# Performance work log

Hardware: AMD Instinct MI355X
Metric: run time of the kernel (lower is better)

## Reference

```python
import jax, jax.numpy as jnp
import numpy as np

B, C, F_, T = 32, 2, 1024, 512
CF = C * F_
H = 128  # lstm hidden / embedding dim


def setup_inputs() -> dict:
    key = jax.random.key(0)
    ks = jax.random.split(key, 12)
    s = 0.05
    return {
        "x": jax.random.normal(ks[0], (B, C, F_, T), dtype=jnp.float32),
        "W_fc1": jax.random.normal(ks[1], (H, CF), dtype=jnp.float32) * s,
        "b_fc1": jax.random.normal(ks[2], (H,), dtype=jnp.float32) * s,
        "Wih_f": jax.random.normal(ks[3], (4 * H, H), dtype=jnp.float32) * s,
        "Whh_f": jax.random.normal(ks[4], (4 * H, H), dtype=jnp.float32) * s,
        "b_f": jax.random.normal(ks[5], (4 * H,), dtype=jnp.float32) * s,
        "Wih_b": jax.random.normal(ks[6], (4 * H, H), dtype=jnp.float32) * s,
        "Whh_b": jax.random.normal(ks[7], (4 * H, H), dtype=jnp.float32) * s,
        "b_b": jax.random.normal(ks[8], (4 * H,), dtype=jnp.float32) * s,
        "W_out": jax.random.normal(ks[9], (H, 2 * H), dtype=jnp.float32) * s,
        "b_out": jax.random.normal(ks[10], (H,), dtype=jnp.float32) * s,
    }


def _lstm_scan(x, Wih, Whh, b):
    # x: (L, T, H); recurrence over L (torch treats the (B,128) input as an
    # unbatched sequence of length B), vectorized over the T frames.
    L, Tn, _ = x.shape
    Hn = Whh.shape[1]

    def step(carry, xt):
        h, c = carry  # (T, H)
        z = xt @ Wih.T + h @ Whh.T + b  # (T, 4H)
        i, f, g, o = jnp.split(z, 4, axis=-1)
        c = jax.nn.sigmoid(f) * c + jax.nn.sigmoid(i) * jnp.tanh(g)
        h = jax.nn.sigmoid(o) * jnp.tanh(c)
        return (h, c), h

    init = (jnp.zeros((Tn, Hn), x.dtype), jnp.zeros((Tn, Hn), x.dtype))
    _, hs = jax.lax.scan(step, init, x)
    return hs  # (L, T, H)


def reference(x, W_fc1, b_fc1, Wih_f, Whh_f, b_f, Wih_b, Whh_b, b_b, W_out, b_out):
    Bn, Cn, Fn, Tn = x.shape
    # fc1 applied per time frame: (B, CF, T) -> (B, T, 128)
    xr = x.reshape(Bn, Cn * Fn, Tn).transpose(0, 2, 1)
    h = jnp.einsum("btc,dc->btd", xr, W_fc1) + b_fc1
    # bidirectional LSTM over the batch axis (torch unbatched-input semantics)
    hf = _lstm_scan(h, Wih_f, Whh_f, b_f)
    hb = _lstm_scan(h[::-1], Wih_b, Whh_b, b_b)[::-1]
    hs = jnp.concatenate([hf, hb], axis=-1)  # (B, T, 256)
    out = jnp.einsum("btd,ed->bte", hs, W_out) + b_out  # (B, T, 128)
    return out.transpose(0, 2, 1)  # (B, 128, T), matching torch.stack(dim=2)
```

## Files before the change

kernel.cpp:

```cpp
#include <hip/hip_runtime.h>
#include <stdint.h>

typedef __attribute__((ext_vector_type(8))) short short8;
typedef __attribute__((ext_vector_type(4))) float floatx4;

__device__ __forceinline__ float bf16_to_f(uint16_t u) {
    union { uint32_t i; float f; } v; v.i = ((uint32_t)u) << 16; return v.f;
}
__device__ __forceinline__ uint16_t f_to_bf16(float f) {
    union { uint32_t i; float f; } v; v.f = f;
    uint32_t u = v.i;
    u += 0x7FFFu + ((u >> 16) & 1u);
    return (uint16_t)(u >> 16);
}
__device__ __forceinline__ void gload16(const void* g, void* l) {
    __builtin_amdgcn_global_load_lds(
        (const __attribute__((address_space(1))) void*)g,
        (__attribute__((address_space(3))) void*)l, 16, 0, 0);
}
__device__ __forceinline__ float rcpf(float x) { return __builtin_amdgcn_rcpf(x); }

#define B_  32
#define T_  512
#define CF_ 2048
#define H_  128
#define G4_ 512
#define LOG2E 1.4426950408889634f

__device__ __forceinline__ void gemm64(const uint16_t* __restrict__ A,
                                       const uint16_t* __restrict__ B,
                                       int K, uint16_t* As, uint16_t* Bs,
                                       floatx4 acc[2][2]) {
    const int tid = threadIdx.x, w = tid >> 6, l = tid & 63;
    const int wm = (w >> 1) * 32, wn = (w & 1) * 32;
    const int lm = l & 15, lk = l >> 4;
    const uint16_t* gA = A + (size_t)l * K;
    const uint16_t* gB = B + (size_t)l * K;
    uint16_t* dA0 = As + ((2 * w) * 64 + l) * 8;
    uint16_t* dA1 = As + ((2 * w + 1) * 64 + l) * 8;
    uint16_t* dB0 = Bs + ((2 * w) * 64 + l) * 8;
    uint16_t* dB1 = Bs + ((2 * w + 1) * 64 + l) * 8;
    for (int k0 = 0; k0 < K; k0 += 64) {
        __syncthreads();
        gload16(gA + k0 + (2 * w) * 8,     dA0);
        gload16(gA + k0 + (2 * w + 1) * 8, dA1);
        gload16(gB + k0 + (2 * w) * 8,     dB0);
        gload16(gB + k0 + (2 * w + 1) * 8, dB1);
        __syncthreads();
        short8 a[2][2], b[2][2];
        #pragma unroll
        for (int kf = 0; kf < 2; ++kf) {
            #pragma unroll
            for (int mf = 0; mf < 2; ++mf)
                a[mf][kf] = *(const short8*)&As[(size_t)((kf * 4 + lk) * 64 + wm + mf * 16 + lm) * 8];
            #pragma unroll
            for (int nf = 0; nf < 2; ++nf)
                b[nf][kf] = *(const short8*)&Bs[(size_t)((kf * 4 + lk) * 64 + wn + nf * 16 + lm) * 8];
        }
        #pragma unroll
        for (int mf = 0; mf < 2; ++mf)
            #pragma unroll
            for (int nf = 0; nf < 2; ++nf) {
                acc[mf][nf] = __builtin_amdgcn_mfma_f32_16x16x32_bf16(a[mf][0], b[nf][0], acc[mf][nf], 0, 0, 0);
                acc[mf][nf] = __builtin_amdgcn_mfma_f32_16x16x32_bf16(a[mf][1], b[nf][1], acc[mf][nf], 0, 0, 0);
            }
    }
}

__global__ __launch_bounds__(256) void k_cvt_all(
        const float* __restrict__ Wfc, const float* __restrict__ Wih_f,
        const float* __restrict__ Wih_b, const float* __restrict__ Whh_f,
        const float* __restrict__ Whh_b, const float* __restrict__ Wout,
        uint16_t* __restrict__ WfcB, uint16_t* __restrict__ WihB,
        uint16_t* __restrict__ WhhB, uint16_t* __restrict__ WoutB) {
    const int blk = blockIdx.x;
    const float* s; uint16_t* d; int off;
    if (blk < 256)      { s = Wfc;   d = WfcB;          off = blk; }
    else if (blk < 320) { s = Wih_f; d = WihB;          off = blk - 256; }
    else if (blk < 384) { s = Wih_b; d = WihB + 65536;  off = blk - 320; }
    else if (blk < 448) { s = Whh_f; d = WhhB;          off = blk - 384; }
    else if (blk < 512) { s = Whh_b; d = WhhB + 65536;  off = blk - 448; }
    else                { s = Wout;  d = WoutB;         off = blk - 512; }
    const int i = off * 1024 + threadIdx.x * 4;
    float4 v = *(const float4*)&s[i];
    ushort4 o;
    o.x = f_to_bf16(v.x); o.y = f_to_bf16(v.y);
    o.z = f_to_bf16(v.z); o.w = f_to_bf16(v.w);
    *(ushort4*)&d[i] = o;
}

__global__ __launch_bounds__(256) void k_xt(const float* __restrict__ x,
                                            uint16_t* __restrict__ xT) {
    __shared__ float tile[64][65];
    const int b = blockIdx.z, cf0 = blockIdx.y * 64, t0 = blockIdx.x * 64;
    const int tid = threadIdx.x;
    #pragma unroll
    for (int p = 0; p < 4; ++p) {
        int cf_r = p * 16 + (tid >> 4);
        int t4   = (tid & 15) * 4;
        float4 v = *(const float4*)&x[((size_t)b * CF_ + cf0 + cf_r) * T_ + t0 + t4];
        tile[t4 + 0][cf_r] = v.x; tile[t4 + 1][cf_r] = v.y;
        tile[t4 + 2][cf_r] = v.z; tile[t4 + 3][cf_r] = v.w;
    }
    __syncthreads();
    #pragma unroll
    for (int p = 0; p < 4; ++p) {
        int t_r = p * 16 + (tid >> 4);
        int cf4 = (tid & 15) * 4;
        ushort4 o;
        o.x = f_to_bf16(tile[t_r][cf4 + 0]);
        o.y = f_to_bf16(tile[t_r][cf4 + 1]);
        o.z = f_to_bf16(tile[t_r][cf4 + 2]);
        o.w = f_to_bf16(tile[t_r][cf4 + 3]);
        *(ushort4*)&xT[((size_t)b * T_ + t0 + t_r) * CF_ + cf0 + cf4] = o;
    }
}

__global__ __launch_bounds__(256) void k_fc1m(const uint16_t* __restrict__ Wb,
                                              const uint16_t* __restrict__ xT,
                                              const float* __restrict__ bfc,
                                              uint16_t* __restrict__ Hfc) {
    __shared__ __align__(16) uint16_t As[4096], Bs[4096];
    const int b = blockIdx.z, m0 = blockIdx.y * 64, n0 = blockIdx.x * 64;
    floatx4 acc[2][2] = {};
    gemm64(Wb + (size_t)m0 * CF_, xT + ((size_t)b * T_ + n0) * CF_, CF_, As, Bs, acc);
    const int tid = threadIdx.x, w = tid >> 6, l = tid & 63;
    const int wm = (w >> 1) * 32, wn = (w & 1) * 32, lm = l & 15, lk = l >> 4;
    #pragma unroll
    for (int mf = 0; mf < 2; ++mf) {
        const int d0 = m0 + wm + mf * 16 + lk * 4;
        const float4 bv = *(const float4*)&bfc[d0];
        #pragma unroll
        for (int nf = 0; nf < 2; ++nf) {
            const int t = n0 + wn + nf * 16 + lm;
            ushort4 o;
            o.x = f_to_bf16(acc[mf][nf][0] + bv.x);
            o.y = f_to_bf16(acc[mf][nf][1] + bv.y);
            o.z = f_to_bf16(acc[mf][nf][2] + bv.z);
            o.w = f_to_bf16(acc[mf][nf][3] + bv.w);
            *(ushort4*)&Hfc[((size_t)b * T_ + t) * H_ + d0] = o;
        }
    }
}

__global__ __launch_bounds__(256) void k_xprojm(const uint16_t* __restrict__ WihB,
                                                const float* __restrict__ b_f,
                                                const float* __restrict__ b_b,
                                                const uint16_t* __restrict__ Hfc,
                                                uint16_t* __restrict__ Xp) {
    __shared__ __align__(16) uint16_t As[4096], Bs[4096];
    const int db = blockIdx.z, dir = db >> 5, b = db & 31;
    const int g0 = blockIdx.y * 64, n0 = blockIdx.x * 64;
    const float* bi = dir ? b_b : b_f;
    floatx4 acc[2][2] = {};
    gemm64(WihB + ((size_t)dir * G4_ + g0) * H_, Hfc + ((size_t)b * T_ + n0) * H_, H_, As, Bs, acc);
    const int tid = threadIdx.x, w = tid >> 6, l = tid & 63;
    const int wm = (w >> 1) * 32, wn = (w & 1) * 32, lm = l & 15, lk = l >> 4;
    #pragma unroll
    for (int mf = 0; mf < 2; ++mf) {
        const int g_ = g0 + wm + mf * 16 + lk * 4;
        const float4 bv = *(const float4*)&bi[g_];
        #pragma unroll
        for (int nf = 0; nf < 2; ++nf) {
            const int t = n0 + wn + nf * 16 + lm;
            ushort4 o;
            o.x = f_to_bf16(acc[mf][nf][0] + bv.x);
            o.y = f_to_bf16(acc[mf][nf][1] + bv.y);
            o.z = f_to_bf16(acc[mf][nf][2] + bv.z);
            o.w = f_to_bf16(acc[mf][nf][3] + bv.w);
            *(ushort4*)&Xp[((size_t)db * T_ + t) * G4_ + g_] = o;
        }
    }
}

__global__ __launch_bounds__(512) void k_lstm(const uint16_t* __restrict__ Xp,
                                              const uint16_t* __restrict__ WhhB,
                                              uint16_t* __restrict__ hs) {
    __shared__ __align__(16) uint16_t h_sh[16 * 136];
    __shared__ float z_sh[16 * 516];
    const int dir = blockIdx.y, t0 = blockIdx.x * 16;
    const int tid = threadIdx.x, w = tid >> 6, l = tid & 63;
    const int lm = l & 15, lk = l >> 4;
    const int gw = w * 64;
    const uint16_t* Wp = WhhB + dir * (G4_ * H_);

    short8 bw[4][4];
    #pragma unroll
    for (int nf = 0; nf < 4; ++nf)
        #pragma unroll
        for (int kf = 0; kf < 4; ++kf)
            bw[nf][kf] = *(const short8*)&Wp[(size_t)(gw + nf * 16 + lm) * H_ + kf * 32 + lk * 8];

    for (int i = tid; i < 16 * 136; i += 512) h_sh[i] = 0;
    const int hh = tid & 127, tq = tid >> 7;
    float c[4] = {0.f, 0.f, 0.f, 0.f};
    __syncthreads();

    for (int s = 0; s < 32; ++s) {
        const int b_idx = dir ? (31 - s) : s;
        const uint16_t* xp = Xp + ((size_t)(dir * B_ + b_idx) * T_ + t0) * G4_;
        uint16_t xv[4][4];
        #pragma unroll
        for (int j = 0; j < 4; ++j)
            #pragma unroll
            for (int gg = 0; gg < 4; ++gg)
                xv[j][gg] = xp[(size_t)(tq * 4 + j) * G4_ + gg * H_ + hh];

        short8 af[4];
        #pragma unroll
        for (int kf = 0; kf < 4; ++kf)
            af[kf] = *(const short8*)&h_sh[lm * 136 + kf * 32 + lk * 8];
        floatx4 acc[4] = {};
        #pragma unroll
        for (int nf = 0; nf < 4; ++nf)
            #pragma unroll
            for (int kf = 0; kf < 4; ++kf)
                acc[nf] = __builtin_amdgcn_mfma_f32_16x16x32_bf16(af[kf], bw[nf][kf], acc[nf], 0, 0, 0);
        #pragma unroll
        for (int nf = 0; nf < 4; ++nf)
            #pragma unroll
            for (int r = 0; r < 4; ++r)
                z_sh[(lk * 4 + r) * 516 + gw + nf * 16 + lm] = acc[nf][r];
        __syncthreads();

        #pragma unroll
        for (int j = 0; j < 4; ++j) {
            const int t = tq * 4 + j;
            const float* zr = &z_sh[t * 516];
            float zi = zr[hh]            + bf16_to_f(xv[j][0]);
            float zf = zr[H_ + hh]       + bf16_to_f(xv[j][1]);
            float zg = zr[2 * H_ + hh]   + bf16_to_f(xv[j][2]);
            float zo = zr[3 * H_ + hh]   + bf16_to_f(xv[j][3]);
            float si = rcpf(1.f + __builtin_amdgcn_exp2f(-LOG2E * zi));
            float sf = rcpf(1.f + __builtin_amdgcn_exp2f(-LOG2E * zf));
            float so = rcpf(1.f + __builtin_amdgcn_exp2f(-LOG2E * zo));
            float tg = 1.f - 2.f * rcpf(1.f + __builtin_amdgcn_exp2f(2.f * LOG2E * zg));
            c[j] = sf * c[j] + si * tg;
            float tc = 1.f - 2.f * rcpf(1.f + __builtin_amdgcn_exp2f(2.f * LOG2E * c[j]));
            float hn = so * tc;
            uint16_t hb = f_to_bf16(hn);
            h_sh[t * 136 + hh] = hb;
            hs[((size_t)b_idx * T_ + t0 + t) * 256 + dir * H_ + hh] = hb;
        }
        __syncthreads();
    }
}

__global__ __launch_bounds__(256) void k_outm(const uint16_t* __restrict__ WoutB,
                                              const uint16_t* __restrict__ hs,
                                              const float* __restrict__ bout,
                                              float* __restrict__ out) {
    __shared__ __align__(16) uint16_t As[4096], Bs[4096];
    const int b = blockIdx.z, m0 = blockIdx.y * 64, n0 = blockIdx.x * 64;
    floatx4 acc[2][2] = {};
    gemm64(WoutB + (size_t)m0 * 256, hs + ((size_t)b * T_ + n0) * 256, 256, As, Bs, acc);
    const int tid = threadIdx.x, w = tid >> 6, l = tid & 63;
    const int wm = (w >> 1) * 32, wn = (w & 1) * 32, lm = l & 15, lk = l >> 4;
    #pragma unroll
    for (int mf = 0; mf < 2; ++mf) {
        const int e0 = m0 + wm + mf * 16 + lk * 4;
        const float4 bv = *(const float4*)&bout[e0];
        #pragma unroll
        for (int nf = 0; nf < 2; ++nf) {
            const int t = n0 + wn + nf * 16 + lm;
            out[((size_t)b * H_ + e0 + 0) * T_ + t] = acc[mf][nf][0] + bv.x;
            out[((size_t)b * H_ + e0 + 1) * T_ + t] = acc[mf][nf][1] + bv.y;
            out[((size_t)b * H_ + e0 + 2) * T_ + t] = acc[mf][nf][2] + bv.z;
            out[((size_t)b * H_ + e0 + 3) * T_ + t] = acc[mf][nf][3] + bv.w;
        }
    }
}

extern "C" void kernel_launch(void* const* d_in, const int* in_sizes, int n_in,
                              void* d_out, int out_size, void* d_ws, size_t ws_size,
                              hipStream_t stream) {
    const float* x     = (const float*)d_in[0];
    const float* Wfc   = (const float*)d_in[1];
    const float* bfc   = (const float*)d_in[2];
    const float* Wih_f = (const float*)d_in[3];
    const float* Whh_f = (const float*)d_in[4];
    const float* b_f   = (const float*)d_in[5];
    const float* Wih_b = (const float*)d_in[6];
    const float* Whh_b = (const float*)d_in[7];
    const float* b_b   = (const float*)d_in[8];
    const float* Wout  = (const float*)d_in[9];
    const float* bout  = (const float*)d_in[10];
    float* out = (float*)d_out;

    char* ws = (char*)d_ws;
    uint16_t* xT    = (uint16_t*)(ws);
    uint16_t* HfcB  = (uint16_t*)(ws + 67108864);
    uint16_t* Xp    = (uint16_t*)(ws + 75497472);
    uint16_t* hsB   = (uint16_t*)(ws + 109051904);
    uint16_t* WfcB  = (uint16_t*)(ws + 117440512);
    uint16_t* WihB  = (uint16_t*)(ws + 117964800);
    uint16_t* WhhB  = (uint16_t*)(ws + 118226944);
    uint16_t* WoutB = (uint16_t*)(ws + 118489088);

    k_cvt_all<<<dim3(544), 256, 0, stream>>>(Wfc, Wih_f, Wih_b, Whh_f, Whh_b, Wout,
                                             WfcB, WihB, WhhB, WoutB);
    k_xt    <<<dim3(8, 32, 32), 256, 0, stream>>>(x, xT);
    k_fc1m  <<<dim3(8, 2, 32),  256, 0, stream>>>(WfcB, xT, bfc, HfcB);
    k_xprojm<<<dim3(8, 8, 64),  256, 0, stream>>>(WihB, b_f, b_b, HfcB, Xp);
    k_lstm  <<<dim3(32, 2),     512, 0, stream>>>(Xp, WhhB, hsB);
    k_outm  <<<dim3(8, 2, 32),  256, 0, stream>>>(WoutB, hsB, bout, out);
}
```

Before: 341.6 us.

## Fuse x transpose, fc1 GEMM and LSTM input projection into one kernel

```diff
diff --git a/kernel.cpp b/kernel.cpp
--- a/kernel.cpp
+++ b/kernel.cpp
@@ -26,46 +26,6 @@
 #define H_  128
 #define G4_ 512
 #define LOG2E 1.4426950408889634f
-
-__device__ __forceinline__ void gemm64(const uint16_t* __restrict__ A,
-                                       const uint16_t* __restrict__ B,
-                                       int K, uint16_t* As, uint16_t* Bs,
-                                       floatx4 acc[2][2]) {
-    const int tid = threadIdx.x, w = tid >> 6, l = tid & 63;
-    const int wm = (w >> 1) * 32, wn = (w & 1) * 32;
-    const int lm = l & 15, lk = l >> 4;
-    const uint16_t* gA = A + (size_t)l * K;
-    const uint16_t* gB = B + (size_t)l * K;
-    uint16_t* dA0 = As + ((2 * w) * 64 + l) * 8;
-    uint16_t* dA1 = As + ((2 * w + 1) * 64 + l) * 8;
-    uint16_t* dB0 = Bs + ((2 * w) * 64 + l) * 8;
-    uint16_t* dB1 = Bs + ((2 * w + 1) * 64 + l) * 8;
-    for (int k0 = 0; k0 < K; k0 += 64) {
-        __syncthreads();
-        gload16(gA + k0 + (2 * w) * 8,     dA0);
-        gload16(gA + k0 + (2 * w + 1) * 8, dA1);
-        gload16(gB + k0 + (2 * w) * 8,     dB0);
-        gload16(gB + k0 + (2 * w + 1) * 8, dB1);
-        __syncthreads();
-        short8 a[2][2], b[2][2];
-        #pragma unroll
-        for (int kf = 0; kf < 2; ++kf) {
-            #pragma unroll
-            for (int mf = 0; mf < 2; ++mf)
-                a[mf][kf] = *(const short8*)&As[(size_t)((kf * 4 + lk) * 64 + wm + mf * 16 + lm) * 8];
-            #pragma unroll
-            for (int nf = 0; nf < 2; ++nf)
-                b[nf][kf] = *(const short8*)&Bs[(size_t)((kf * 4 + lk) * 64 + wn + nf * 16 + lm) * 8];
-        }
-        #pragma unroll
-        for (int mf = 0; mf < 2; ++mf)
-            #pragma unroll
-            for (int nf = 0; nf < 2; ++nf) {
-                acc[mf][nf] = __builtin_amdgcn_mfma_f32_16x16x32_bf16(a[mf][0], b[nf][0], acc[mf][nf], 0, 0, 0);
-                acc[mf][nf] = __builtin_amdgcn_mfma_f32_16x16x32_bf16(a[mf][1], b[nf][1], acc[mf][nf], 0, 0, 0);
-            }
-    }
-}
 
 __global__ __launch_bounds__(256) void k_cvt_all(
         const float* __restrict__ Wfc, const float* __restrict__ Wih_f,
@@ -89,86 +49,141 @@
     *(ushort4*)&d[i] = o;
 }
 
-__global__ __launch_bounds__(256) void k_xt(const float* __restrict__ x,
-                                            uint16_t* __restrict__ xT) {
-    __shared__ float tile[64][65];
-    const int b = blockIdx.z, cf0 = blockIdx.y * 64, t0 = blockIdx.x * 64;
-    const int tid = threadIdx.x;
-    #pragma unroll
-    for (int p = 0; p < 4; ++p) {
-        int cf_r = p * 16 + (tid >> 4);
-        int t4   = (tid & 15) * 4;
-        float4 v = *(const float4*)&x[((size_t)b * CF_ + cf0 + cf_r) * T_ + t0 + t4];
-        tile[t4 + 0][cf_r] = v.x; tile[t4 + 1][cf_r] = v.y;
-        tile[t4 + 2][cf_r] = v.z; tile[t4 + 3][cf_r] = v.w;
+__global__ __launch_bounds__(512) void k_fc1x(const float* __restrict__ x,
+                                              const uint16_t* __restrict__ WfcB,
+                                              const float* __restrict__ bfc,
+                                              const uint16_t* __restrict__ WihB,
+                                              const float* __restrict__ b_f,
+                                              const float* __restrict__ b_b,
+                                              uint16_t* __restrict__ Xp) {
+    __shared__ float tile[64 * 65];
+    __shared__ __align__(16) uint16_t As[8192];
+    __shared__ __align__(16) uint16_t Bs[4224];
+    __shared__ __align__(16) uint16_t Hs2[8432];
+
+    const int bb = blockIdx.y, n0 = blockIdx.x * 64;
+    const int tid = threadIdx.x, w = tid >> 6, l = tid & 63;
+    const int lm = l & 15, lk = l >> 4;
+    const float* xb = x + (size_t)bb * CF_ * T_;
+
+    const int t4 = (tid & 15) * 4, cf_r = tid >> 4;
+    const int kk = (tid & 15) * 4, t_r = tid >> 4;
+
+    float4 xv0, xv1;
+    {
+        const float* p = &xb[(size_t)(0 + cf_r) * T_ + n0 + t4];
+        xv0 = *(const float4*)p;
+        xv1 = *(const float4*)(p + 32 * T_);
+    }
+
+    const int wmA = (w >> 1) * 32, wnA = (w & 1) * 32;
+    floatx4 acc[2][2] = {};
+    for (int k0 = 0; k0 < CF_; k0 += 64) {
+        __syncthreads();
+        tile[(t4 + 0) * 65 + cf_r] = xv0.x;
+        tile[(t4 + 1) * 65 + cf_r] = xv0.y;
+        tile[(t4 + 2) * 65 + cf_r] = xv0.z;
+        tile[(t4 + 3) * 65 + cf_r] = xv0.w;
+        tile[(t4 + 0) * 65 + cf_r + 32] = xv1.x;
+        tile[(t4 + 1) * 65 + cf_r + 32] = xv1.y;
+        tile[(t4 + 2) * 65 + cf_r + 32] = xv1.z;
+        tile[(t4 + 3) * 65 + cf_r + 32] = xv1.w;
+        gload16(WfcB + (size_t)l * CF_ + k0 + w * 8,        As + (w * 128 + l) * 8);
+        gload16(WfcB + (size_t)(64 + l) * CF_ + k0 + w * 8, As + (w * 128 + 64 + l) * 8);
+        __syncthreads();
+        if (k0 + 64 < CF_) {
+            const float* p = &xb[(size_t)(k0 + 64 + cf_r) * T_ + n0 + t4];
+            xv0 = *(const float4*)p;
+            xv1 = *(const float4*)(p + 32 * T_);
+        }
+        #pragma unroll
+        for (int pass = 0; pass < 2; ++pass) {
+            const int tr = t_r + pass * 32;
+            ushort4 o;
+            o.x = f_to_bf16(tile[tr * 65 + kk + 0]);
+            o.y = f_to_bf16(tile[tr * 65 + kk + 1]);
+            o.z = f_to_bf16(tile[tr * 65 + kk + 2]);
+            o.w = f_to_bf16(tile[tr * 65 + kk + 3]);
+            *(ushort4*)&Bs[((kk >> 3) * 66 + tr) * 8 + (kk & 7)] = o;
+        }
+        __syncthreads();
+        short8 a[2][2], bfr[2][2];
+        #pragma unroll
+        for (int kf = 0; kf < 2; ++kf) {
+            #pragma unroll
+            for (int mf = 0; mf < 2; ++mf)
+                a[mf][kf] = *(const short8*)&As[((kf * 4 + lk) * 128 + wmA + mf * 16 + lm) * 8];
+            #pragma unroll
+            for (int nf = 0; nf < 2; ++nf)
+                bfr[nf][kf] = *(const short8*)&Bs[((kf * 4 + lk) * 66 + wnA + nf * 16 + lm) * 8];
+        }
+        #pragma unroll
+        for (int mf = 0; mf < 2; ++mf)
+            #pragma unroll
+            for (int nf = 0; nf < 2; ++nf) {
+                acc[mf][nf] = __builtin_amdgcn_mfma_f32_16x16x32_bf16(a[mf][0], bfr[nf][0], acc[mf][nf], 0, 0, 0);
+                acc[mf][nf] = __builtin_amdgcn_mfma_f32_16x16x32_bf16(a[mf][1], bfr[nf][1], acc[mf][nf], 0, 0, 0);
+            }
     }
     __syncthreads();
     #pragma unroll
-    for (int p = 0; p < 4; ++p) {
-        int t_r = p * 16 + (tid >> 4);
-        int cf4 = (tid & 15) * 4;
-        ushort4 o;
-        o.x = f_to_bf16(tile[t_r][cf4 + 0]);
-        o.y = f_to_bf16(tile[t_r][cf4 + 1]);
-        o.z = f_to_bf16(tile[t_r][cf4 + 2]);
-        o.w = f_to_bf16(tile[t_r][cf4 + 3]);
-        *(ushort4*)&xT[((size_t)b * T_ + t0 + t_r) * CF_ + cf0 + cf4] = o;
-    }
-}
-
-__global__ __launch_bounds__(256) void k_fc1m(const uint16_t* __restrict__ Wb,
-                                              const uint16_t* __restrict__ xT,
-                                              const float* __restrict__ bfc,
-                                              uint16_t* __restrict__ Hfc) {
-    __shared__ __align__(16) uint16_t As[4096], Bs[4096];
-    const int b = blockIdx.z, m0 = blockIdx.y * 64, n0 = blockIdx.x * 64;
-    floatx4 acc[2][2] = {};
-    gemm64(Wb + (size_t)m0 * CF_, xT + ((size_t)b * T_ + n0) * CF_, CF_, As, Bs, acc);
-    const int tid = threadIdx.x, w = tid >> 6, l = tid & 63;
-    const int wm = (w >> 1) * 32, wn = (w & 1) * 32, lm = l & 15, lk = l >> 4;
-    #pragma unroll
     for (int mf = 0; mf < 2; ++mf) {
-        const int d0 = m0 + wm + mf * 16 + lk * 4;
+        const int d0 = wmA + mf * 16 + lk * 4;
         const float4 bv = *(const float4*)&bfc[d0];
+        const int c = ((wmA + mf * 16) >> 3) + (lk >> 1);
         #pragma unroll
         for (int nf = 0; nf < 2; ++nf) {
-            const int t = n0 + wn + nf * 16 + lm;
+            const int t = wnA + nf * 16 + lm;
             ushort4 o;
             o.x = f_to_bf16(acc[mf][nf][0] + bv.x);
             o.y = f_to_bf16(acc[mf][nf][1] + bv.y);
             o.z = f_to_bf16(acc[mf][nf][2] + bv.z);
             o.w = f_to_bf16(acc[mf][nf][3] + bv.w);
-            *(ushort4*)&Hfc[((size_t)b * T_ + t) * H_ + d0] = o;
-        }
-    }
-}
-
-__global__ __launch_bounds__(256) void k_xprojm(const uint16_t* __restrict__ WihB,
-                                                const float* __restrict__ b_f,
-                                                const float* __restrict__ b_b,
-                                                const uint16_t* __restrict__ Hfc,
-                                                uint16_t* __restrict__ Xp) {
-    __shared__ __align__(16) uint16_t As[4096], Bs[4096];
-    const int db = blockIdx.z, dir = db >> 5, b = db & 31;
-    const int g0 = blockIdx.y * 64, n0 = blockIdx.x * 64;
-    const float* bi = dir ? b_b : b_f;
-    floatx4 acc[2][2] = {};
-    gemm64(WihB + ((size_t)dir * G4_ + g0) * H_, Hfc + ((size_t)b * T_ + n0) * H_, H_, As, Bs, acc);
-    const int tid = threadIdx.x, w = tid >> 6, l = tid & 63;
-    const int wm = (w >> 1) * 32, wn = (w & 1) * 32, lm = l & 15, lk = l >> 4;
+            *(ushort4*)&Hs2[(c * 66 + t) * 8 + (lk & 1) * 4] = o;
+        }
+    }
+    __syncthreads();
+
+    const int dirw = w >> 2;
+    const int db   = dirw * B_ + bb;
+    const uint16_t* Wp = WihB + (size_t)dirw * (G4_ * H_);
+    const float* bi = dirw ? b_b : b_f;
     #pragma unroll
-    for (int mf = 0; mf < 2; ++mf) {
-        const int g_ = g0 + wm + mf * 16 + lk * 4;
-        const float4 bv = *(const float4*)&bi[g_];
-        #pragma unroll
-        for (int nf = 0; nf < 2; ++nf) {
-            const int t = n0 + wn + nf * 16 + lm;
-            ushort4 o;
-            o.x = f_to_bf16(acc[mf][nf][0] + bv.x);
-            o.y = f_to_bf16(acc[mf][nf][1] + bv.y);
-            o.z = f_to_bf16(acc[mf][nf][2] + bv.z);
-            o.w = f_to_bf16(acc[mf][nf][3] + bv.w);
-            *(ushort4*)&Xp[((size_t)db * T_ + t) * G4_ + g_] = o;
+    for (int it = 0; it < 2; ++it) {
+        const int gbase = (w & 3) * 64 + it * 256;
+        short8 aw[4][4];
+        #pragma unroll
+        for (int mf = 0; mf < 4; ++mf)
+            #pragma unroll
+            for (int kf = 0; kf < 4; ++kf)
+                aw[mf][kf] = *(const short8*)&Wp[(size_t)(gbase + mf * 16 + lm) * H_ + kf * 32 + lk * 8];
+        floatx4 acc2[4][4] = {};
+        #pragma unroll
+        for (int nf = 0; nf < 4; ++nf) {
+            short8 bbf[4];
+            #pragma unroll
+            for (int kf = 0; kf < 4; ++kf)
+                bbf[kf] = *(const short8*)&Hs2[((kf * 4 + lk) * 66 + nf * 16 + lm) * 8];
+            #pragma unroll
+            for (int mf = 0; mf < 4; ++mf)
+                #pragma unroll
+                for (int kf = 0; kf < 4; ++kf)
+                    acc2[mf][nf] = __builtin_amdgcn_mfma_f32_16x16x32_bf16(aw[mf][kf], bbf[kf], acc2[mf][nf], 0, 0, 0);
+        }
+        #pragma unroll
+        for (int mf = 0; mf < 4; ++mf) {
+            const int g0 = gbase + mf * 16 + lk * 4;
+            const float4 bv = *(const float4*)&bi[g0];
+            #pragma unroll
+            for (int nf = 0; nf < 4; ++nf) {
+                const int t = n0 + nf * 16 + lm;
+                ushort4 o;
+                o.x = f_to_bf16(acc2[mf][nf][0] + bv.x);
+                o.y = f_to_bf16(acc2[mf][nf][1] + bv.y);
+                o.z = f_to_bf16(acc2[mf][nf][2] + bv.z);
+                o.w = f_to_bf16(acc2[mf][nf][3] + bv.w);
+                *(ushort4*)&Xp[((size_t)db * T_ + t) * G4_ + g0] = o;
+            }
         }
     }
 }
@@ -252,10 +267,39 @@
                                               float* __restrict__ out) {
     __shared__ __align__(16) uint16_t As[4096], Bs[4096];
     const int b = blockIdx.z, m0 = blockIdx.y * 64, n0 = blockIdx.x * 64;
+    const int tid = threadIdx.x, w = tid >> 6, l = tid & 63;
+    const int wm = (w >> 1) * 32, wn = (w & 1) * 32;
+    const int lm = l & 15, lk = l >> 4;
+    const uint16_t* A = WoutB + (size_t)m0 * 256;
+    const uint16_t* Bp = hs + ((size_t)b * T_ + n0) * 256;
     floatx4 acc[2][2] = {};
-    gemm64(WoutB + (size_t)m0 * 256, hs + ((size_t)b * T_ + n0) * 256, 256, As, Bs, acc);
-    const int tid = threadIdx.x, w = tid >> 6, l = tid & 63;
-    const int wm = (w >> 1) * 32, wn = (w & 1) * 32, lm = l & 15, lk = l >> 4;
+    const uint16_t* gA = A + (size_t)l * 256;
+    const uint16_t* gB = Bp + (size_t)l * 256;
+    for (int k0 = 0; k0 < 256; k0 += 64) {
+        __syncthreads();
+        gload16(gA + k0 + (2 * w) * 8,     As + ((2 * w) * 64 + l) * 8);
+        gload16(gA + k0 + (2 * w + 1) * 8, As + ((2 * w + 1) * 64 + l) * 8);
+        gload16(gB + k0 + (2 * w) * 8,     Bs + ((2 * w) * 64 + l) * 8);
+        gload16(gB + k0 + (2 * w + 1) * 8, Bs + ((2 * w + 1) * 64 + l) * 8);
+        __syncthreads();
+        short8 a[2][2], bfr[2][2];
+        #pragma unroll
+        for (int kf = 0; kf < 2; ++kf) {
+            #pragma unroll
+            for (int mf = 0; mf < 2; ++mf)
+                a[mf][kf] = *(const short8*)&As[((kf * 4 + lk) * 64 + wm + mf * 16 + lm) * 8];
+            #pragma unroll
+            for (int nf = 0; nf < 2; ++nf)
+                bfr[nf][kf] = *(const short8*)&Bs[((kf * 4 + lk) * 64 + wn + nf * 16 + lm) * 8];
+        }
+        #pragma unroll
+        for (int mf = 0; mf < 2; ++mf)
+            #pragma unroll
+            for (int nf = 0; nf < 2; ++nf) {
+                acc[mf][nf] = __builtin_amdgcn_mfma_f32_16x16x32_bf16(a[mf][0], bfr[nf][0], acc[mf][nf], 0, 0, 0);
+                acc[mf][nf] = __builtin_amdgcn_mfma_f32_16x16x32_bf16(a[mf][1], bfr[nf][1], acc[mf][nf], 0, 0, 0);
+            }
+    }
     #pragma unroll
     for (int mf = 0; mf < 2; ++mf) {
         const int e0 = m0 + wm + mf * 16 + lk * 4;
@@ -288,20 +332,16 @@
     float* out = (float*)d_out;
 
     char* ws = (char*)d_ws;
-    uint16_t* xT    = (uint16_t*)(ws);
-    uint16_t* HfcB  = (uint16_t*)(ws + 67108864);
-    uint16_t* Xp    = (uint16_t*)(ws + 75497472);
-    uint16_t* hsB   = (uint16_t*)(ws + 109051904);
-    uint16_t* WfcB  = (uint16_t*)(ws + 117440512);
-    uint16_t* WihB  = (uint16_t*)(ws + 117964800);
-    uint16_t* WhhB  = (uint16_t*)(ws + 118226944);
-    uint16_t* WoutB = (uint16_t*)(ws + 118489088);
+    uint16_t* Xp    = (uint16_t*)(ws);
+    uint16_t* hsB   = (uint16_t*)(ws + 33554432);
+    uint16_t* WfcB  = (uint16_t*)(ws + 41943040);
+    uint16_t* WihB  = (uint16_t*)(ws + 42467328);
+    uint16_t* WhhB  = (uint16_t*)(ws + 42729472);
+    uint16_t* WoutB = (uint16_t*)(ws + 42991616);
 
     k_cvt_all<<<dim3(544), 256, 0, stream>>>(Wfc, Wih_f, Wih_b, Whh_f, Whh_b, Wout,
                                              WfcB, WihB, WhhB, WoutB);
-    k_xt    <<<dim3(8, 32, 32), 256, 0, stream>>>(x, xT);
-    k_fc1m  <<<dim3(8, 2, 32),  256, 0, stream>>>(WfcB, xT, bfc, HfcB);
-    k_xprojm<<<dim3(8, 8, 64),  256, 0, stream>>>(WihB, b_f, b_b, HfcB, Xp);
-    k_lstm  <<<dim3(32, 2),     512, 0, stream>>>(Xp, WhhB, hsB);
-    k_outm  <<<dim3(8, 2, 32),  256, 0, stream>>>(WoutB, hsB, bout, out);
-}
+    k_fc1x <<<dim3(8, 32),   512, 0, stream>>>(x, WfcB, bfc, WihB, b_f, b_b, Xp);
+    k_lstm <<<dim3(32, 2),   512, 0, stream>>>(Xp, WhhB, hsB);
+    k_outm <<<dim3(8, 2, 32), 256, 0, stream>>>(WoutB, hsB, bout, out);
+}
```

Result: faster. 298.9 us (-12.5%).
